# Kernel tuning notes

Hardware: AMD Instinct MI355X
Metric: run time of the kernel (lower is better)

The kernel has to match this reference:

```python
import jax, jax.numpy as jnp
import numpy as np

N_USERS = 100000
N_ITEMS = 200000
N_TOTAL = N_USERS + N_ITEMS
N_EDGES = 6000000
D = 64


def setup_inputs() -> dict:
    key = jax.random.key(0)
    ks = jax.random.split(key, 7)
    A_row = jax.random.randint(ks[0], (N_EDGES,), 0, N_TOTAL, dtype=jnp.int32)
    A_col = jax.random.randint(ks[1], (N_EDGES,), 0, N_TOTAL, dtype=jnp.int32)
    A_val = jax.random.uniform(ks[2], (N_EDGES,), dtype=jnp.float32)
    user_feat = jax.random.normal(ks[3], (N_USERS, D), dtype=jnp.float32)
    item_feat = jax.random.normal(ks[4], (N_ITEMS, D), dtype=jnp.float32)
    W = jax.random.normal(ks[5], (D, D), dtype=jnp.float32) * (6.0 / (D + D)) ** 0.5
    b = jnp.zeros((D,), dtype=jnp.float32)
    return {"A_row": A_row, "A_col": A_col, "A_val": A_val,
            "user_feat": user_feat, "item_feat": item_feat, "W": W, "b": b}


def reference(A_row, A_col, A_val, user_feat, item_feat, W, b):
    # fc applied to users and items (same weight), then concat -> [N_total, D]
    all_feat = jnp.concatenate([user_feat, item_feat], axis=0)
    trans = all_feat @ W.T + b  # nn.Linear: x @ W^T + b
    # sparse A (COO) @ trans: gather source rows, scale by edge value, scatter-add to dest
    msgs = A_val[:, None] * trans[A_col]  # [E, D]
    conv = jax.ops.segment_sum(msgs, A_row, num_segments=N_TOTAL)  # [N_total, D]
    # identity residual (in_dim == out_dim)
    out = conv + all_feat
    return out[:N_USERS], out[N_USERS:]
```

## Files before the change

### kernel.cpp

```cpp
#include <hip/hip_runtime.h>
#include <hip/hip_fp16.h>

#define N_USERS 100000
#define N_ITEMS 200000
#define N_TOTAL 300000
#define N_EDGES 6000000
#define D 64

#define B2SHIFT 9
#define B2ROWS 512
#define NBUCK2 ((N_TOTAL + B2ROWS - 1) / B2ROWS)
#define CAP 11264
#define EPB 8192
#define NPB ((N_EDGES + EPB - 1) / EPB)
#define GPAD 16

#define VSCALE 8191.0f
#define VINV   (1.0f / 8191.0f)

typedef float    f32x4 __attribute__((ext_vector_type(4)));
typedef float    f32x2 __attribute__((ext_vector_type(2)));
typedef _Float16 f16x8 __attribute__((ext_vector_type(8)));

#define LIN_BLOCKS ((N_TOTAL + 63) / 64)

__global__ __launch_bounds__(256) void fused_lin_part_kernel(
    const float* __restrict__ user_feat,
    const float* __restrict__ item_feat,
    const float* __restrict__ W,
    const float* __restrict__ bias,
    __half* __restrict__ trans,
    const int*   __restrict__ A_row,
    const int*   __restrict__ A_col,
    const float* __restrict__ A_val,
    int*  __restrict__ gcur,
    int2* __restrict__ kv)
{
    if (blockIdx.x < NPB) {
        __shared__ int lcnt[NBUCK2];
        __shared__ int gb[NBUCK2];
        for (int i = threadIdx.x; i < NBUCK2; i += 256) lcnt[i] = 0;
        __syncthreads();

        const int base = blockIdx.x * EPB;
        int pk[32];
        #pragma unroll
        for (int j = 0; j < 8; ++j) {
            const int e0 = base + j * 1024 + threadIdx.x * 4;
            if (e0 < N_EDGES) {
                const int4 r = *reinterpret_cast<const int4*>(A_row + e0);
                pk[4*j+0] = ((r.x >> B2SHIFT) << 13) | atomicAdd(&lcnt[r.x >> B2SHIFT], 1);
                pk[4*j+1] = ((r.y >> B2SHIFT) << 13) | atomicAdd(&lcnt[r.y >> B2SHIFT], 1);
                pk[4*j+2] = ((r.z >> B2SHIFT) << 13) | atomicAdd(&lcnt[r.z >> B2SHIFT], 1);
                pk[4*j+3] = ((r.w >> B2SHIFT) << 13) | atomicAdd(&lcnt[r.w >> B2SHIFT], 1);
            }
        }
        __syncthreads();
        for (int i = threadIdx.x; i < NBUCK2; i += 256)
            gb[i] = lcnt[i] ? atomicAdd(&gcur[(size_t)i * GPAD], lcnt[i]) : 0;
        __syncthreads();

        #pragma unroll
        for (int j = 0; j < 8; ++j) {
            const int e0 = base + j * 1024 + threadIdx.x * 4;
            if (e0 < N_EDGES) {
                const int4   r = *reinterpret_cast<const int4*>(A_row + e0);
                const int4   c = *reinterpret_cast<const int4*>(A_col + e0);
                const float4 v = *reinterpret_cast<const float4*>(A_val + e0);
                const int rr[4] = {r.x, r.y, r.z, r.w};
                const int cc[4] = {c.x, c.y, c.z, c.w};
                const float vv[4] = {v.x, v.y, v.z, v.w};
                #pragma unroll
                for (int q = 0; q < 4; ++q) {
                    const int p   = pk[4*j+q];
                    const int bk  = p >> 13;
                    const int pos = gb[bk] + (p & 0x1FFF);
                    if (pos < CAP) {
                        kv[(size_t)bk * CAP + pos] = make_int2(
                            ((rr[q] & (B2ROWS - 1)) << 19) | cc[q],
                            __float_as_int(vv[q]));
                    }
                }
            }
        }
    } else {
        const int bid  = blockIdx.x - NPB;
        const int lane = threadIdx.x & 63;
        const int wv   = threadIdx.x >> 6;
        const int r0   = bid * 64 + wv * 16;
        const int arow = lane & 15;
        const int kg   = lane >> 4;

        f16x8 wf[4][2];
        #pragma unroll
        for (int ct = 0; ct < 4; ++ct) {
            const float* wp = W + (size_t)(ct * 16 + arow) * D;
            #pragma unroll
            for (int kf = 0; kf < 2; ++kf) {
                const int k0 = kf * 32 + kg * 8;
                const float4 w0 = *reinterpret_cast<const float4*>(wp + k0);
                const float4 w1 = *reinterpret_cast<const float4*>(wp + k0 + 4);
                f16x8 h;
                h[0] = (_Float16)w0.x; h[1] = (_Float16)w0.y;
                h[2] = (_Float16)w0.z; h[3] = (_Float16)w0.w;
                h[4] = (_Float16)w1.x; h[5] = (_Float16)w1.y;
                h[6] = (_Float16)w1.z; h[7] = (_Float16)w1.w;
                wf[ct][kf] = h;
            }
        }

        int rr = r0 + arow;
        if (rr >= N_TOTAL) rr = N_TOTAL - 1;
        const float* fp = (rr < N_USERS) ? user_feat + (size_t)rr * D
                                         : item_feat + (size_t)(rr - N_USERS) * D;
        f16x8 af[2];
        #pragma unroll
        for (int kf = 0; kf < 2; ++kf) {
            const int k0 = kf * 32 + kg * 8;
            const float4 a0 = *reinterpret_cast<const float4*>(fp + k0);
            const float4 a1 = *reinterpret_cast<const float4*>(fp + k0 + 4);
            f16x8 h;
            h[0] = (_Float16)a0.x; h[1] = (_Float16)a0.y;
            h[2] = (_Float16)a0.z; h[3] = (_Float16)a0.w;
            h[4] = (_Float16)a1.x; h[5] = (_Float16)a1.y;
            h[6] = (_Float16)a1.z; h[7] = (_Float16)a1.w;
            af[kf] = h;
        }

        #pragma unroll
        for (int ct = 0; ct < 4; ++ct) {
            const float bc = bias[ct * 16 + arow];
            f32x4 acc = {bc, bc, bc, bc};
            acc = __builtin_amdgcn_mfma_f32_16x16x32_f16(af[0], wf[ct][0], acc, 0, 0, 0);
            acc = __builtin_amdgcn_mfma_f32_16x16x32_f16(af[1], wf[ct][1], acc, 0, 0, 0);
            #pragma unroll
            for (int reg = 0; reg < 4; ++reg) {
                const int ro = r0 + kg * 4 + reg;
                if (ro < N_TOTAL)
                    trans[(size_t)ro * D + ct * 16 + arow] = __float2half(acc[reg]);
            }
        }
    }
}

__global__ __launch_bounds__(512) void bucket_csr3_kernel(
    const int*  __restrict__ gcur,
    const int2* __restrict__ kv,
    int* __restrict__ rowoff,
    int* __restrict__ outp)
{
    __shared__ int rcnt[B2ROWS];
    __shared__ int rcur[B2ROWS];
    __shared__ int s[512];
    const int b    = blockIdx.x;
    const int t    = threadIdx.x;
    const int n    = min(gcur[(size_t)b * GPAD], CAP);
    const int base = b * CAP;

    rcnt[t] = 0;
    __syncthreads();
    for (int i = t; i < n; i += 512)
        atomicAdd(&rcnt[kv[base + i].x >> 19], 1);
    __syncthreads();

    const int v0 = rcnt[t];
    s[t] = v0;
    __syncthreads();
    for (int d2 = 1; d2 < 512; d2 <<= 1) {
        const int x = (t >= d2) ? s[t - d2] : 0;
        __syncthreads();
        s[t] += x;
        __syncthreads();
    }
    rcur[t] = s[t] - v0;
    __syncthreads();

    for (int i = t; i < n; i += 512) {
        const int2 e = kv[base + i];
        const int  p = atomicAdd(&rcur[e.x >> 19], 1);
        const int  q = (int)fminf(fmaxf(__int_as_float(e.y) * VSCALE + 0.5f, 0.0f), VSCALE);
        outp[base + p] = (q << 19) | (e.x & 0x7FFFF);
    }
    __syncthreads();

    const int row = (b << B2SHIFT) + t;
    if (row < N_TOTAL) rowoff[row] = base + rcur[t];
}

__global__ __launch_bounds__(256) void pull5_kernel(
    const int*    __restrict__ rowoff,
    const int*    __restrict__ outp,
    const __half* __restrict__ trans,
    const float*  __restrict__ user_feat,
    const float*  __restrict__ item_feat,
    float* __restrict__ out)
{
    const int lane = threadIdx.x & 63;
    const int row  = blockIdx.x * 4 + (threadIdx.x >> 6);
    if (row >= N_TOTAL) return;
    const int g  = lane >> 3;
    const int l8 = lane & 7;

    const int s0 = ((row & (B2ROWS - 1)) == 0) ? (row >> B2SHIFT) * CAP
                                               : rowoff[row - 1];
    const int e  = rowoff[row];

    f32x2 a0 = {0.f, 0.f}, a1 = {0.f, 0.f}, a2 = {0.f, 0.f}, a3 = {0.f, 0.f};

    for (int bi = s0; bi < e; bi += 8) {
        const int i = bi + g;
        if (i < e) {
            const int k = outp[i];
            const float w = (float)((unsigned)k >> 19) * VINV;
            const f32x2 w2 = {w, w};
            const float4 gv = *reinterpret_cast<const float4*>(
                trans + ((size_t)(k & 0x7FFFF) << 6) + 8 * l8);
            const float2 f0 = __half22float2(*reinterpret_cast<const __half2*>(&gv.x));
            const float2 f1 = __half22float2(*reinterpret_cast<const __half2*>(&gv.y));
            const float2 f2 = __half22float2(*reinterpret_cast<const __half2*>(&gv.z));
            const float2 f3 = __half22float2(*reinterpret_cast<const __half2*>(&gv.w));
            a0 += w2 * (f32x2){f0.x, f0.y};
            a1 += w2 * (f32x2){f1.x, f1.y};
            a2 += w2 * (f32x2){f2.x, f2.y};
            a3 += w2 * (f32x2){f3.x, f3.y};
        }
    }

    #pragma unroll
    for (int d2 = 8; d2 <= 32; d2 <<= 1) {
        a0[0] += __shfl_xor(a0[0], d2); a0[1] += __shfl_xor(a0[1], d2);
        a1[0] += __shfl_xor(a1[0], d2); a1[1] += __shfl_xor(a1[1], d2);
        a2[0] += __shfl_xor(a2[0], d2); a2[1] += __shfl_xor(a2[1], d2);
        a3[0] += __shfl_xor(a3[0], d2); a3[1] += __shfl_xor(a3[1], d2);
    }

    if (g == 0) {
        const float* fp = (row < N_USERS)
            ? user_feat + ((size_t)row << 6)
            : item_feat + ((size_t)(row - N_USERS) << 6);
        const float4 r0 = *reinterpret_cast<const float4*>(fp + 8 * l8);
        const float4 r1 = *reinterpret_cast<const float4*>(fp + 8 * l8 + 4);
        float* op = out + ((size_t)row << 6) + 8 * l8;
        *reinterpret_cast<float4*>(op) =
            make_float4(a0[0] + r0.x, a0[1] + r0.y, a1[0] + r0.z, a1[1] + r0.w);
        *reinterpret_cast<float4*>(op + 4) =
            make_float4(a2[0] + r1.x, a2[1] + r1.y, a3[0] + r1.z, a3[1] + r1.w);
    }
}

__global__ __launch_bounds__(256) void linear_kernel(
    const float* __restrict__ user_feat,
    const float* __restrict__ item_feat,
    const float* __restrict__ W,
    const float* __restrict__ b,
    float* __restrict__ trans,
    float* __restrict__ out)
{
    __shared__ float Ws[D][D + 1];
    __shared__ float bs[D];
    const int t = threadIdx.x;
    for (int i = t; i < D * D; i += 256) Ws[i >> 6][i & 63] = W[i];
    if (t < D) bs[t] = b[t];
    __syncthreads();

    const int lane = t & 63;
    const int row  = blockIdx.x * 4 + (t >> 6);
    if (row >= N_TOTAL) return;

    const float* feat = (row < N_USERS)
        ? user_feat + (size_t)row * D
        : item_feat + (size_t)(row - N_USERS) * D;

    const float fv = feat[lane];
    float acc = bs[lane];
    #pragma unroll
    for (int k = 0; k < D; ++k)
        acc = fmaf(__shfl(fv, k, 64), Ws[lane][k], acc);

    const size_t off = (size_t)row * D + lane;
    trans[off] = acc;
    if (out) out[off] = fv;
}

__global__ __launch_bounds__(256) void edge_scatter_kernel(
    const int*   __restrict__ A_row,
    const int*   __restrict__ A_col,
    const float* __restrict__ A_val,
    const float* __restrict__ trans,
    float*       __restrict__ out)
{
    const int lane = threadIdx.x & 63;
    const long long e = ((long long)blockIdx.x * 256 + threadIdx.x) >> 6;
    if (e >= N_EDGES) return;
    atomicAdd(out + (size_t)A_row[e] * D + lane,
              A_val[e] * trans[(size_t)A_col[e] * D + lane]);
}

__global__ __launch_bounds__(256) void init_out_kernel(
    const float* __restrict__ user_feat,
    const float* __restrict__ item_feat,
    float* __restrict__ out)
{
    const size_t i = (size_t)blockIdx.x * 256 + threadIdx.x;
    if (i >= (size_t)N_TOTAL * D) return;
    const size_t urows = (size_t)N_USERS * D;
    out[i] = (i < urows) ? user_feat[i] : item_feat[i - urows];
}

__global__ __launch_bounds__(256) void fused_edge_kernel(
    const int*   __restrict__ A_row,
    const int*   __restrict__ A_col,
    const float* __restrict__ A_val,
    const float* __restrict__ user_feat,
    const float* __restrict__ item_feat,
    const float* __restrict__ W,
    const float* __restrict__ b,
    float*       __restrict__ out)
{
    __shared__ float Ws[D][D + 1];
    __shared__ float bs[D];
    const int t = threadIdx.x;
    for (int i = t; i < D * D; i += 256) Ws[i >> 6][i & 63] = W[i];
    if (t < D) bs[t] = b[t];
    __syncthreads();

    const int lane = t & 63;
    const long long e = ((long long)blockIdx.x * 256 + t) >> 6;
    if (e >= N_EDGES) return;

    const int   r = A_row[e];
    const int   c = A_col[e];
    const float v = A_val[e];

    const float* feat = (c < N_USERS)
        ? user_feat + (size_t)c * D
        : item_feat + (size_t)(c - N_USERS) * D;

    const float fv = feat[lane];
    float acc = bs[lane];
    #pragma unroll
    for (int k = 0; k < D; ++k)
        acc = fmaf(__shfl(fv, k, 64), Ws[lane][k], acc);

    atomicAdd(out + (size_t)r * D + lane, v * acc);
}

extern "C" void kernel_launch(void* const* d_in, const int* in_sizes, int n_in,
                              void* d_out, int out_size, void* d_ws, size_t ws_size,
                              hipStream_t stream)
{
    const int*   A_row     = (const int*)  d_in[0];
    const int*   A_col     = (const int*)  d_in[1];
    const float* A_val     = (const float*)d_in[2];
    const float* user_feat = (const float*)d_in[3];
    const float* item_feat = (const float*)d_in[4];
    const float* W         = (const float*)d_in[5];
    const float* b         = (const float*)d_in[6];
    float*       out       = (float*)d_out;

    const size_t a256 = 255;
    const size_t transh_bytes = (((size_t)N_TOTAL * D * sizeof(__half)) + a256) & ~a256;
    const size_t gcur_bytes   = (((size_t)NBUCK2 * GPAD * sizeof(int)) + a256) & ~a256;
    const size_t kv_bytes     = (((size_t)NBUCK2 * CAP * sizeof(int2)) + a256) & ~a256;
    const size_t rowoff_bytes = (((size_t)N_TOTAL * sizeof(int)) + a256) & ~a256;
    const size_t outp_bytes   = (((size_t)NBUCK2 * CAP * sizeof(int)) + a256) & ~a256;
    const size_t main_total   = transh_bytes + gcur_bytes + kv_bytes
                              + rowoff_bytes + outp_bytes;

    const size_t trans_bytes  = (size_t)N_TOTAL * D * sizeof(float);

    const int row_blocks = (N_TOTAL + 3) / 4;

    if (ws_size >= main_total) {
        char* p = (char*)d_ws;
        __half* transh = (__half*)p;  p += transh_bytes;
        int*    gcur   = (int*)p;     p += gcur_bytes;
        int2*   kv     = (int2*)p;    p += kv_bytes;
        int*    rowoff = (int*)p;     p += rowoff_bytes;
        int*    outp   = (int*)p;

        hipMemsetAsync(gcur, 0, (size_t)NBUCK2 * GPAD * sizeof(int), stream);
        fused_lin_part_kernel<<<NPB + LIN_BLOCKS, 256, 0, stream>>>(
            user_feat, item_feat, W, b, transh,
            A_row, A_col, A_val, gcur, kv);
        bucket_csr3_kernel<<<NBUCK2, 512, 0, stream>>>(
            gcur, kv, rowoff, outp);
        pull5_kernel<<<row_blocks, 256, 0, stream>>>(
            rowoff, outp, transh, user_feat, item_feat, out);
    } else if (ws_size >= trans_bytes) {
        float* trans = (float*)d_ws;
        linear_kernel<<<row_blocks, 256, 0, stream>>>(
            user_feat, item_feat, W, b, trans, out);
        edge_scatter_kernel<<<N_EDGES / 4, 256, 0, stream>>>(
            A_row, A_col, A_val, trans, out);
    } else {
        const size_t total = (size_t)N_TOTAL * D;
        init_out_kernel<<<(int)((total + 255) / 256), 256, 0, stream>>>(
            user_feat, item_feat, out);
        fused_edge_kernel<<<N_EDGES / 4, 256, 0, stream>>>(
            A_row, A_col, A_val, user_feat, item_feat, W, b, out);
    }
}
```

Before: 395.3 us.

## Fuse CSR build and pull into per-bucket LDS half2 atomic accumulation

The separate per-row CSR sort kernel and the row-pull kernel are replaced by one kernel. It accumulates each 256-row bucket's messages in shared memory with fp16x2 atomic adds, using an XOR swizzle to spread LDS bank use, and then adds the residual and writes the output. The partition kernel now stages edges in LDS sorted by bucket so that global writes to kv are coalesced, and buckets shrink from 512 to 256 rows. This removes one kernel launch and the rowoff/outp round trip through global memory. In exchange, accumulation happens in fp16 with atomics, which risks precision loss and LDS contention, and the partition block now holds a large shared staging buffer.

```diff
diff --git a/kernel.cpp b/kernel.cpp
--- a/kernel.cpp
+++ b/kernel.cpp
@@ -7,19 +7,14 @@
 #define N_EDGES 6000000
 #define D 64
 
-#define B2SHIFT 9
-#define B2ROWS 512
-#define NBUCK2 ((N_TOTAL + B2ROWS - 1) / B2ROWS)
-#define CAP 11264
-#define EPB 8192
+#define B3SHIFT 8
+#define B3ROWS 256
+#define NBUCK3 ((N_TOTAL + B3ROWS - 1) / B3ROWS)
+#define CAP3 5888
+#define EPB 4096
 #define NPB ((N_EDGES + EPB - 1) / EPB)
-#define GPAD 16
-
-#define VSCALE 8191.0f
-#define VINV   (1.0f / 8191.0f)
 
 typedef float    f32x4 __attribute__((ext_vector_type(4)));
-typedef float    f32x2 __attribute__((ext_vector_type(2)));
 typedef _Float16 f16x8 __attribute__((ext_vector_type(8)));
 
 #define LIN_BLOCKS ((N_TOTAL + 63) / 64)
@@ -36,51 +31,92 @@
     int*  __restrict__ gcur,
     int2* __restrict__ kv)
 {
+    __shared__ int  lcnt[NBUCK3];
+    __shared__ int  gb[NBUCK3];
+    __shared__ int  loff[NBUCK3];
+    __shared__ int  s[256];
+    __shared__ int2 stage[EPB];
+
     if (blockIdx.x < NPB) {
-        __shared__ int lcnt[NBUCK2];
-        __shared__ int gb[NBUCK2];
-        for (int i = threadIdx.x; i < NBUCK2; i += 256) lcnt[i] = 0;
+        const int t = threadIdx.x;
+        for (int i = t; i < NBUCK3; i += 256) lcnt[i] = 0;
         __syncthreads();
 
         const int base = blockIdx.x * EPB;
-        int pk[32];
-        #pragma unroll
-        for (int j = 0; j < 8; ++j) {
-            const int e0 = base + j * 1024 + threadIdx.x * 4;
+        int pk[16];
+        #pragma unroll
+        for (int j = 0; j < 4; ++j) {
+            const int e0 = base + j * 1024 + t * 4;
             if (e0 < N_EDGES) {
                 const int4 r = *reinterpret_cast<const int4*>(A_row + e0);
-                pk[4*j+0] = ((r.x >> B2SHIFT) << 13) | atomicAdd(&lcnt[r.x >> B2SHIFT], 1);
-                pk[4*j+1] = ((r.y >> B2SHIFT) << 13) | atomicAdd(&lcnt[r.y >> B2SHIFT], 1);
-                pk[4*j+2] = ((r.z >> B2SHIFT) << 13) | atomicAdd(&lcnt[r.z >> B2SHIFT], 1);
-                pk[4*j+3] = ((r.w >> B2SHIFT) << 13) | atomicAdd(&lcnt[r.w >> B2SHIFT], 1);
-            }
-        }
-        __syncthreads();
-        for (int i = threadIdx.x; i < NBUCK2; i += 256)
-            gb[i] = lcnt[i] ? atomicAdd(&gcur[(size_t)i * GPAD], lcnt[i]) : 0;
-        __syncthreads();
-
-        #pragma unroll
-        for (int j = 0; j < 8; ++j) {
-            const int e0 = base + j * 1024 + threadIdx.x * 4;
+                pk[4*j+0] = ((r.x >> B3SHIFT) << 13) | atomicAdd(&lcnt[r.x >> B3SHIFT], 1);
+                pk[4*j+1] = ((r.y >> B3SHIFT) << 13) | atomicAdd(&lcnt[r.y >> B3SHIFT], 1);
+                pk[4*j+2] = ((r.z >> B3SHIFT) << 13) | atomicAdd(&lcnt[r.z >> B3SHIFT], 1);
+                pk[4*j+3] = ((r.w >> B3SHIFT) << 13) | atomicAdd(&lcnt[r.w >> B3SHIFT], 1);
+            }
+        }
+        __syncthreads();
+
+        int v[5]; int sum = 0;
+        #pragma unroll
+        for (int q = 0; q < 5; ++q) {
+            const int idx = t * 5 + q;
+            v[q] = (idx < NBUCK3) ? lcnt[idx] : 0;
+            sum += v[q];
+        }
+        s[t] = sum;
+        __syncthreads();
+        for (int d2 = 1; d2 < 256; d2 <<= 1) {
+            const int x = (t >= d2) ? s[t - d2] : 0;
+            __syncthreads();
+            s[t] += x;
+            __syncthreads();
+        }
+        int run = (t == 0) ? 0 : s[t - 1];
+        #pragma unroll
+        for (int q = 0; q < 5; ++q) {
+            const int idx = t * 5 + q;
+            if (idx < NBUCK3) loff[idx] = run;
+            run += v[q];
+        }
+        __syncthreads();
+        for (int i = t; i < NBUCK3; i += 256)
+            gb[i] = lcnt[i] ? atomicAdd(&gcur[i], lcnt[i]) : 0;
+        __syncthreads();
+
+        #pragma unroll
+        for (int j = 0; j < 4; ++j) {
+            const int e0 = base + j * 1024 + t * 4;
             if (e0 < N_EDGES) {
                 const int4   r = *reinterpret_cast<const int4*>(A_row + e0);
                 const int4   c = *reinterpret_cast<const int4*>(A_col + e0);
-                const float4 v = *reinterpret_cast<const float4*>(A_val + e0);
+                const float4 vv4 = *reinterpret_cast<const float4*>(A_val + e0);
                 const int rr[4] = {r.x, r.y, r.z, r.w};
                 const int cc[4] = {c.x, c.y, c.z, c.w};
-                const float vv[4] = {v.x, v.y, v.z, v.w};
+                const float vl[4] = {vv4.x, vv4.y, vv4.z, vv4.w};
                 #pragma unroll
                 for (int q = 0; q < 4; ++q) {
-                    const int p   = pk[4*j+q];
-                    const int bk  = p >> 13;
-                    const int pos = gb[bk] + (p & 0x1FFF);
-                    if (pos < CAP) {
-                        kv[(size_t)bk * CAP + pos] = make_int2(
-                            ((rr[q] & (B2ROWS - 1)) << 19) | cc[q],
-                            __float_as_int(vv[q]));
-                    }
+                    const int p  = pk[4*j+q];
+                    const int bk = p >> 13;
+                    stage[loff[bk] + (p & 0x1FFF)] = make_int2(
+                        ((rr[q] & (B3ROWS - 1)) << 19) | cc[q],
+                        __float_as_int(vl[q]));
                 }
+            }
+        }
+        __syncthreads();
+
+        const int wv   = t >> 6;
+        const int lane = t & 63;
+        for (int b2 = wv; b2 < NBUCK3; b2 += 4) {
+            const int len = lcnt[b2];
+            if (!len) continue;
+            const int st    = loff[b2];
+            const int gbase = gb[b2];
+            int2* dst = kv + (size_t)b2 * CAP3;
+            for (int j = lane; j < len; j += 64) {
+                const int pos = gbase + j;
+                if (pos < CAP3) dst[pos] = stage[st + j];
             }
         }
     } else {
@@ -143,108 +179,75 @@
     }
 }
 
-__global__ __launch_bounds__(512) void bucket_csr3_kernel(
-    const int*  __restrict__ gcur,
-    const int2* __restrict__ kv,
-    int* __restrict__ rowoff,
-    int* __restrict__ outp)
-{
-    __shared__ int rcnt[B2ROWS];
-    __shared__ int rcur[B2ROWS];
-    __shared__ int s[512];
-    const int b    = blockIdx.x;
-    const int t    = threadIdx.x;
-    const int n    = min(gcur[(size_t)b * GPAD], CAP);
-    const int base = b * CAP;
-
-    rcnt[t] = 0;
-    __syncthreads();
-    for (int i = t; i < n; i += 512)
-        atomicAdd(&rcnt[kv[base + i].x >> 19], 1);
-    __syncthreads();
-
-    const int v0 = rcnt[t];
-    s[t] = v0;
-    __syncthreads();
-    for (int d2 = 1; d2 < 512; d2 <<= 1) {
-        const int x = (t >= d2) ? s[t - d2] : 0;
-        __syncthreads();
-        s[t] += x;
-        __syncthreads();
-    }
-    rcur[t] = s[t] - v0;
-    __syncthreads();
-
-    for (int i = t; i < n; i += 512) {
-        const int2 e = kv[base + i];
-        const int  p = atomicAdd(&rcur[e.x >> 19], 1);
-        const int  q = (int)fminf(fmaxf(__int_as_float(e.y) * VSCALE + 0.5f, 0.0f), VSCALE);
-        outp[base + p] = (q << 19) | (e.x & 0x7FFFF);
-    }
-    __syncthreads();
-
-    const int row = (b << B2SHIFT) + t;
-    if (row < N_TOTAL) rowoff[row] = base + rcur[t];
-}
-
-__global__ __launch_bounds__(256) void pull5_kernel(
-    const int*    __restrict__ rowoff,
-    const int*    __restrict__ outp,
+__global__ __launch_bounds__(512) void bucket_acc_pull_kernel(
+    const int*    __restrict__ gcur,
+    const int2*   __restrict__ kv,
     const __half* __restrict__ trans,
     const float*  __restrict__ user_feat,
     const float*  __restrict__ item_feat,
     float* __restrict__ out)
 {
-    const int lane = threadIdx.x & 63;
-    const int row  = blockIdx.x * 4 + (threadIdx.x >> 6);
-    if (row >= N_TOTAL) return;
-    const int g  = lane >> 3;
-    const int l8 = lane & 7;
-
-    const int s0 = ((row & (B2ROWS - 1)) == 0) ? (row >> B2SHIFT) * CAP
-                                               : rowoff[row - 1];
-    const int e  = rowoff[row];
-
-    f32x2 a0 = {0.f, 0.f}, a1 = {0.f, 0.f}, a2 = {0.f, 0.f}, a3 = {0.f, 0.f};
-
-    for (int bi = s0; bi < e; bi += 8) {
-        const int i = bi + g;
-        if (i < e) {
-            const int k = outp[i];
-            const float w = (float)((unsigned)k >> 19) * VINV;
-            const f32x2 w2 = {w, w};
-            const float4 gv = *reinterpret_cast<const float4*>(
-                trans + ((size_t)(k & 0x7FFFF) << 6) + 8 * l8);
-            const float2 f0 = __half22float2(*reinterpret_cast<const __half2*>(&gv.x));
-            const float2 f1 = __half22float2(*reinterpret_cast<const __half2*>(&gv.y));
-            const float2 f2 = __half22float2(*reinterpret_cast<const __half2*>(&gv.z));
-            const float2 f3 = __half22float2(*reinterpret_cast<const __half2*>(&gv.w));
-            a0 += w2 * (f32x2){f0.x, f0.y};
-            a1 += w2 * (f32x2){f1.x, f1.y};
-            a2 += w2 * (f32x2){f2.x, f2.y};
-            a3 += w2 * (f32x2){f3.x, f3.y};
-        }
+    __shared__ __half2 acc[B3ROWS][D / 2];
+    const int b = blockIdx.x;
+    const int t = threadIdx.x;
+
+    int* az = reinterpret_cast<int*>(acc);
+    for (int i = t; i < B3ROWS * (D / 2); i += 512) az[i] = 0;
+    __syncthreads();
+
+    const int n = min(gcur[b], CAP3);
+    const int2* seg = kv + (size_t)b * CAP3;
+    const int wv   = t >> 6;
+    const int lane = t & 63;
+    const int g    = lane >> 3;
+    const int l8   = lane & 7;
+    __half2* accf = &acc[0][0];
+
+    for (int i = wv * 8 + g; i < n; i += 128) {
+        const int  i1 = i + 64;
+        const int2 kA = seg[i];
+        const int2 kB = (i1 < n) ? seg[i1] : make_int2(0, 0);
+
+        const int lrA = ((unsigned)kA.x) >> 19, colA = kA.x & 0x7FFFF;
+        const int lrB = ((unsigned)kB.x) >> 19, colB = kB.x & 0x7FFFF;
+
+        const float4 gA = *reinterpret_cast<const float4*>(
+            trans + ((size_t)colA << 6) + 8 * l8);
+        const float4 gB = *reinterpret_cast<const float4*>(
+            trans + ((size_t)colB << 6) + 8 * l8);
+
+        const __half2 wA = __float2half2_rn(__int_as_float(kA.y));
+        const __half2 wB = __float2half2_rn(__int_as_float(kB.y));
+
+        const __half2* hA = reinterpret_cast<const __half2*>(&gA);
+        const __half2* hB = reinterpret_cast<const __half2*>(&gB);
+        const int oA = lrA * 32 + ((l8 ^ (lrA & 7)) << 2);
+        const int oB = lrB * 32 + ((l8 ^ (lrB & 7)) << 2);
+        #pragma unroll
+        for (int jj = 0; jj < 4; ++jj)
+            unsafeAtomicAdd(&accf[oA + jj], __hmul2(wA, hA[jj]));
+        #pragma unroll
+        for (int jj = 0; jj < 4; ++jj)
+            unsafeAtomicAdd(&accf[oB + jj], __hmul2(wB, hB[jj]));
     }
-
-    #pragma unroll
-    for (int d2 = 8; d2 <= 32; d2 <<= 1) {
-        a0[0] += __shfl_xor(a0[0], d2); a0[1] += __shfl_xor(a0[1], d2);
-        a1[0] += __shfl_xor(a1[0], d2); a1[1] += __shfl_xor(a1[1], d2);
-        a2[0] += __shfl_xor(a2[0], d2); a2[1] += __shfl_xor(a2[1], d2);
-        a3[0] += __shfl_xor(a3[0], d2); a3[1] += __shfl_xor(a3[1], d2);
-    }
-
-    if (g == 0) {
+    __syncthreads();
+
+    const int rbase = b << B3SHIFT;
+    for (int rr = wv * 2; rr < B3ROWS; rr += 16) {
+        const int lr  = rr + (lane >> 5);
+        const int row = rbase + lr;
+        if (row >= N_TOTAL) continue;
+        const int h  = lane & 31;
+        const int o  = h >> 2, jj = h & 3;
+        const int o0 = o ^ (lr & 7);
+        const int c0 = o0 * 8 + jj * 2;
+        const float2 f = __half22float2(acc[lr][h]);
         const float* fp = (row < N_USERS)
             ? user_feat + ((size_t)row << 6)
             : item_feat + ((size_t)(row - N_USERS) << 6);
-        const float4 r0 = *reinterpret_cast<const float4*>(fp + 8 * l8);
-        const float4 r1 = *reinterpret_cast<const float4*>(fp + 8 * l8 + 4);
-        float* op = out + ((size_t)row << 6) + 8 * l8;
-        *reinterpret_cast<float4*>(op) =
-            make_float4(a0[0] + r0.x, a0[1] + r0.y, a1[0] + r0.z, a1[1] + r0.w);
-        *reinterpret_cast<float4*>(op + 4) =
-            make_float4(a2[0] + r1.x, a2[1] + r1.y, a3[0] + r1.z, a3[1] + r1.w);
+        const float2 r2 = *reinterpret_cast<const float2*>(fp + c0);
+        *reinterpret_cast<float2*>(out + ((size_t)row << 6) + c0) =
+            make_float2(f.x + r2.x, f.y + r2.y);
     }
 }
 
@@ -360,12 +363,9 @@
 
     const size_t a256 = 255;
     const size_t transh_bytes = (((size_t)N_TOTAL * D * sizeof(__half)) + a256) & ~a256;
-    const size_t gcur_bytes   = (((size_t)NBUCK2 * GPAD * sizeof(int)) + a256) & ~a256;
-    const size_t kv_bytes     = (((size_t)NBUCK2 * CAP * sizeof(int2)) + a256) & ~a256;
-    const size_t rowoff_bytes = (((size_t)N_TOTAL * sizeof(int)) + a256) & ~a256;
-    const size_t outp_bytes   = (((size_t)NBUCK2 * CAP * sizeof(int)) + a256) & ~a256;
-    const size_t main_total   = transh_bytes + gcur_bytes + kv_bytes
-                              + rowoff_bytes + outp_bytes;
+    const size_t gcur_bytes   = (((size_t)NBUCK3 * sizeof(int)) + a256) & ~a256;
+    const size_t kv_bytes     = (((size_t)NBUCK3 * CAP3 * sizeof(int2)) + a256) & ~a256;
+    const size_t main_total   = transh_bytes + gcur_bytes + kv_bytes;
 
     const size_t trans_bytes  = (size_t)N_TOTAL * D * sizeof(float);
 
@@ -375,18 +375,14 @@
         char* p = (char*)d_ws;
         __half* transh = (__half*)p;  p += transh_bytes;
         int*    gcur   = (int*)p;     p += gcur_bytes;
-        int2*   kv     = (int2*)p;    p += kv_bytes;
-        int*    rowoff = (int*)p;     p += rowoff_bytes;
-        int*    outp   = (int*)p;
-
-        hipMemsetAsync(gcur, 0, (size_t)NBUCK2 * GPAD * sizeof(int), stream);
+        int2*   kv     = (int2*)p;
+
+        hipMemsetAsync(gcur, 0, (size_t)NBUCK3 * sizeof(int), stream);
         fused_lin_part_kernel<<<NPB + LIN_BLOCKS, 256, 0, stream>>>(
             user_feat, item_feat, W, b, transh,
             A_row, A_col, A_val, gcur, kv);
-        bucket_csr3_kernel<<<NBUCK2, 512, 0, stream>>>(
-            gcur, kv, rowoff, outp);
-        pull5_kernel<<<row_blocks, 256, 0, stream>>>(
-            rowoff, outp, transh, user_feat, item_feat, out);
+        bucket_acc_pull_kernel<<<NBUCK3, 512, 0, stream>>>(
+            gcur, kv, transh, user_feat, item_feat, out);
     } else if (ws_size >= trans_bytes) {
         float* trans = (float*)d_ws;
         linear_kernel<<<row_blocks, 256, 0, stream>>>(
```

After: 1.262 ms. 3.19x slower.
